# Performance work log

Measured on AMD Instinct MI355X. Metric: run time of the kernel, lower is better.

Reference implementation:

```python
import jax, jax.numpy as jnp
import numpy as np

DIM = 1024
HEADS = 16
DIM_HEAD = 64
INNER = HEADS * DIM_HEAD  # 1024
B, N = 2, 2048


def setup_inputs() -> dict:
    key = jax.random.key(0)
    ks = jax.random.split(key, 8)
    q = jax.random.normal(ks[0], (B, N, DIM), dtype=jnp.float32)
    k = jax.random.normal(ks[1], (B, N, DIM), dtype=jnp.float32)
    v = jax.random.normal(ks[2], (B, N, DIM), dtype=jnp.float32)
    # True = masked out (masked_fill semantics); causal mask broadcast over batch
    causal = jnp.triu(jnp.ones((N, N), dtype=jnp.bool_), k=1)
    mask = jnp.broadcast_to(causal, (B, N, N))
    s = 0.02
    Wq = jax.random.normal(ks[3], (DIM, INNER), dtype=jnp.float32) * s
    Wk = jax.random.normal(ks[4], (DIM, INNER), dtype=jnp.float32) * s
    Wv = jax.random.normal(ks[5], (DIM, INNER), dtype=jnp.float32) * s
    Wo = jax.random.normal(ks[6], (INNER, DIM), dtype=jnp.float32) * s
    bo = jnp.zeros((DIM,), dtype=jnp.float32)
    return {"q": q, "k": k, "v": v, "mask": mask,
            "Wq": Wq, "Wk": Wk, "Wv": Wv, "Wo": Wo, "bo": bo}


def reference(q, k, v, mask, Wq, Wk, Wv, Wo, bo):
    h, d = HEADS, DIM_HEAD
    scale = d ** -0.5
    b, n, _ = q.shape

    def heads_split(x):  # [b, n, h*d] -> [b, h, n, d]
        return x.reshape(b, -1, h, d).transpose(0, 2, 1, 3)

    qh = heads_split(q @ Wq)
    kh = heads_split(k @ Wk)
    vh = heads_split(v @ Wv)

    dots = jnp.einsum('bhid,bhjd->bhij', qh, kh) * scale  # [b,h,n,n]
    mask_value = -jnp.finfo(dots.dtype).max
    dots = jnp.where(mask[:, None, :, :], mask_value, dots)
    attn = jax.nn.softmax(dots, axis=-1)
    out = jnp.einsum('bhij,bhjd->bhid', attn, vh)          # [b,h,n,d]
    out = out.transpose(0, 2, 1, 3).reshape(b, n, h * d)    # [b,n,h*d]
    out = out @ Wo + bo                                     # RowParallelLinear (bias=True)
    return out  # dropout p=0.0 is identity
```

## Files before the change

### kernel.cpp

```cpp
#include <hip/hip_runtime.h>

typedef __attribute__((ext_vector_type(8))) short short8;
typedef __attribute__((ext_vector_type(4))) float f32x4;
typedef __attribute__((ext_vector_type(4))) unsigned int u32x4;

#define MFMA_BF16(a, b, c) __builtin_amdgcn_mfma_f32_16x16x32_bf16((a), (b), (c), 0, 0, 0)

#define GLOAD16(g, l) __builtin_amdgcn_global_load_lds( \
    (const __attribute__((address_space(1))) void*)(g),  \
    (__attribute__((address_space(3))) void*)(l), 16, 0, 0)

#define BARRIER() __builtin_amdgcn_s_barrier()
#define LGKMCNT0() do { asm volatile("s_waitcnt lgkmcnt(0)" ::: "memory"); \
                        __builtin_amdgcn_sched_barrier(0); } while (0)
#define VMCNT(n) asm volatile("s_waitcnt vmcnt(" n ")" ::: "memory")

static __device__ __forceinline__ unsigned short f2bf(float f) {
    unsigned int u = __builtin_bit_cast(unsigned int, f);
    u += 0x7fffu + ((u >> 16) & 1u);
    return (unsigned short)(u >> 16);
}
static __device__ __forceinline__ unsigned int cvtpk(float a, float b) {
    unsigned int r;
    asm("v_cvt_pk_bf16_f32 %0, %1, %2" : "=v"(r) : "v"(a), "v"(b));
    return r;
}
static __device__ __forceinline__ float ex2(float x) {
    float r;
    asm("v_exp_f32 %0, %1" : "=v"(r) : "v"(x));
    return r;
}

__global__ __launch_bounds__(256) void convX_kernel(
    const float* __restrict__ q, const float* __restrict__ k, const float* __restrict__ v,
    unsigned short* __restrict__ dq, unsigned short* __restrict__ dk,
    unsigned short* __restrict__ dv)
{
    const float* s; unsigned short* d;
    switch (blockIdx.y) {
        case 0:  s = q; d = dq; break;
        case 1:  s = k; d = dk; break;
        default: s = v; d = dv; break;
    }
    int i = (blockIdx.x * 256 + threadIdx.x) * 8;
    float4 a = *reinterpret_cast<const float4*>(s + i);
    float4 b = *reinterpret_cast<const float4*>(s + i + 4);
    short8 o;
    o[0] = (short)f2bf(a.x); o[1] = (short)f2bf(a.y);
    o[2] = (short)f2bf(a.z); o[3] = (short)f2bf(a.w);
    o[4] = (short)f2bf(b.x); o[5] = (short)f2bf(b.y);
    o[6] = (short)f2bf(b.z); o[7] = (short)f2bf(b.w);
    *reinterpret_cast<short8*>(d + i) = o;
}

__global__ __launch_bounds__(256) void convWT_kernel(
    const float* __restrict__ w0, const float* __restrict__ w1,
    const float* __restrict__ w2, const float* __restrict__ w3,
    unsigned short* __restrict__ t0, unsigned short* __restrict__ t1,
    unsigned short* __restrict__ t2, unsigned short* __restrict__ t3)
{
    const float* W; unsigned short* T;
    switch (blockIdx.z) {
        case 0:  W = w0; T = t0; break;
        case 1:  W = w1; T = t1; break;
        case 2:  W = w2; T = t2; break;
        default: W = w3; T = t3; break;
    }
    __shared__ unsigned short ldsT[64][72];
    const int t = threadIdx.x;
    const int kb = blockIdx.x * 64, cb = blockIdx.y * 64;

    const int c4 = (t & 15) * 4;
    const int r0 = t >> 4;
    #pragma unroll
    for (int i = 0; i < 4; ++i) {
        int kr = r0 + i * 16;
        float4 wv = *reinterpret_cast<const float4*>(&W[(size_t)(kb + kr) * 1024 + cb + c4]);
        ldsT[c4 + 0][kr] = f2bf(wv.x);
        ldsT[c4 + 1][kr] = f2bf(wv.y);
        ldsT[c4 + 2][kr] = f2bf(wv.z);
        ldsT[c4 + 3][kr] = f2bf(wv.w);
    }
    __syncthreads();
    const int c = t >> 2;
    const int kp = (t & 3) * 16;
    short8 o0 = *reinterpret_cast<const short8*>(&ldsT[c][kp]);
    short8 o1 = *reinterpret_cast<const short8*>(&ldsT[c][kp + 8]);
    *reinterpret_cast<short8*>(&T[(size_t)(cb + c) * 1024 + kb + kp])     = o0;
    *reinterpret_cast<short8*>(&T[(size_t)(cb + c) * 1024 + kb + kp + 8]) = o1;
}

__device__ __forceinline__ void gemm_body(
    const unsigned short* __restrict__ A, const unsigned short* __restrict__ B,
    int tm, int cn, unsigned short* Al, unsigned short* Bl, f32x4 acc[4][4])
{
    const int t = threadIdx.x;
    const int lane = t & 63, w = t >> 6;
    const int lr = lane & 15, lg = lane >> 4;
    const int wr = w >> 1, wc = w & 1;

    const int srow = w * 16 + (lane >> 2);
    const int sk   = (lane & 3) * 8;
    const unsigned short* ga = A + (size_t)(tm + srow) * 1024 + sk;
    const unsigned short* gb = B + (size_t)(cn + srow) * 1024 + sk;
    unsigned short* la = Al + srow * 32 + sk;
    unsigned short* lb = Bl + srow * 32 + sk;

    for (int k0 = 0; k0 < 1024; k0 += 32) {
        __syncthreads();
        GLOAD16(ga + k0, la);
        GLOAD16(ga + k0 + (size_t)64 * 1024, la + 64 * 32);
        GLOAD16(gb + k0, lb);
        GLOAD16(gb + k0 + (size_t)64 * 1024, lb + 64 * 32);
        asm volatile("s_waitcnt vmcnt(0)" ::: "memory");
        __syncthreads();

        short8 af[4], bfr[4];
        #pragma unroll
        for (int i = 0; i < 4; ++i) {
            af[i]  = *reinterpret_cast<const short8*>(&Al[(wr * 64 + i * 16 + lr) * 32 + lg * 8]);
            bfr[i] = *reinterpret_cast<const short8*>(&Bl[(wc * 64 + i * 16 + lr) * 32 + lg * 8]);
        }
        #pragma unroll
        for (int mi = 0; mi < 4; ++mi)
            #pragma unroll
            for (int ni = 0; ni < 4; ++ni)
                acc[mi][ni] = MFMA_BF16(af[mi], bfr[ni], acc[mi][ni]);
    }
}

__global__ __launch_bounds__(512, 2) void qkv_gemm(
    const unsigned short* __restrict__ Xq, const unsigned short* __restrict__ Xk,
    const unsigned short* __restrict__ Xv,
    const unsigned short* __restrict__ WqT, const unsigned short* __restrict__ WkT,
    const unsigned short* __restrict__ WvT,
    unsigned short* __restrict__ Qh, unsigned short* __restrict__ Kh,
    unsigned short* __restrict__ VhT)
{
    extern __shared__ unsigned short lds[];
    const int t    = threadIdx.x;
    const int lane = t & 63, w = t >> 6;
    const int lr   = lane & 15, lg = lane >> 4;
    const int wrow = w >> 2, wcol = w & 3;
    const int sw   = lr & 7;

    const int z = blockIdx.z;
    const unsigned short *A, *B; unsigned short* dst;
    int tm, cn;
    if (z == 2)      { A = WvT; B = Xv;  dst = VhT; tm = blockIdx.y * 256; cn = blockIdx.x * 256; }
    else if (z == 1) { A = Xk;  B = WkT; dst = Kh;  tm = blockIdx.x * 256; cn = blockIdx.y * 256; }
    else             { A = Xq;  B = WqT; dst = Qh;  tm = blockIdx.x * 256; cn = blockIdx.y * 256; }

    const unsigned short* Ag = A + (size_t)tm * 1024;
    const unsigned short* Bg = B + (size_t)cn * 1024;

    const int sr    = t >> 3;
    const int gsw   = (t & 7) ^ (sr & 7);
    const int brow0 = (sr >> 5) * 64 + (sr & 31);

    auto stageA = [&](int q, int kt, unsigned short* slabA) {
        const unsigned short* g = Ag + (size_t)(q * 64 + sr) * 1024 + kt + gsw * 8;
        GLOAD16(g, slabA + q * 8192 + t * 8);
        GLOAD16(g + (size_t)128 * 1024, slabA + q * 8192 + 4096 + t * 8);
    };
    auto stageB = [&](int s, int kt, unsigned short* slabB) {
        const unsigned short* g = Bg + (size_t)(brow0 + s * 32) * 1024 + kt + gsw * 8;
        GLOAD16(g, slabB + s * 8192 + t * 8);
        GLOAD16(g + (size_t)128 * 1024, slabB + s * 8192 + 4096 + t * 8);
    };

    short8 rA[4][2], rB0[2][2], rB1[2][2];
    auto ldA = [&](const unsigned short* bufA, int q) {
        #pragma unroll
        for (int m2 = 0; m2 < 4; ++m2) {
            const unsigned short* p = bufA + q * 8192 + (wrow * 64 + m2 * 16 + lr) * 64;
            rA[m2][0] = *reinterpret_cast<const short8*>(p + (lg ^ sw) * 8);
            rA[m2][1] = *reinterpret_cast<const short8*>(p + ((4 + lg) ^ sw) * 8);
        }
    };
    auto ldB = [&](const unsigned short* bufB, int s, short8 rB[2][2]) {
        #pragma unroll
        for (int n2 = 0; n2 < 2; ++n2) {
            const unsigned short* p = bufB + s * 8192 + (wcol * 32 + n2 * 16 + lr) * 64;
            rB[n2][0] = *reinterpret_cast<const short8*>(p + (lg ^ sw) * 8);
            rB[n2][1] = *reinterpret_cast<const short8*>(p + ((4 + lg) ^ sw) * 8);
        }
    };

    f32x4 acc[8][4];
    #pragma unroll
    for (int i = 0; i < 8; ++i)
        #pragma unroll
        for (int j = 0; j < 4; ++j) acc[i][j] = (f32x4){0.f, 0.f, 0.f, 0.f};

#define QUAD(MH, NH, RB) do {                                            \
    _Pragma("unroll")                                                    \
    for (int m2 = 0; m2 < 4; ++m2) {                                     \
        _Pragma("unroll")                                                \
        for (int n2 = 0; n2 < 2; ++n2) {                                 \
            f32x4 c_ = acc[(MH)*4 + m2][(NH)*2 + n2];                    \
            c_ = MFMA_BF16(rA[m2][0], (RB)[n2][0], c_);                  \
            c_ = MFMA_BF16(rA[m2][1], (RB)[n2][1], c_);                  \
            acc[(MH)*4 + m2][(NH)*2 + n2] = c_;                          \
        } } } while (0)

    stageA(0, 0, lds);
    stageB(0, 0, lds + 16384);
    stageB(1, 0, lds + 16384);
    stageA(1, 0, lds);
    VMCNT("4");
    BARRIER();

    for (int tt = 0; tt < 15; ++tt) {
        unsigned short* cA = lds + (tt & 1) * 32768;
        unsigned short* cB = cA + 16384;
        unsigned short* nA = lds + ((tt + 1) & 1) * 32768;
        unsigned short* nB = nA + 16384;
        const int kn = (tt + 1) * 64;
        stageA(0, kn, nA);
        ldA(cA, 0); ldB(cB, 0, rB0);
        VMCNT("4"); BARRIER(); LGKMCNT0();
        __builtin_amdgcn_s_setprio(1); QUAD(0, 0, rB0); __builtin_amdgcn_s_setprio(0);
        BARRIER();
        stageB(0, kn, nB);
        ldB(cB, 1, rB1);
        VMCNT("4"); BARRIER(); LGKMCNT0();
        __builtin_amdgcn_s_setprio(1); QUAD(0, 1, rB1); __builtin_amdgcn_s_setprio(0);
        BARRIER();
        stageB(1, kn, nB);
        ldA(cA, 1);
        BARRIER(); LGKMCNT0();
        __builtin_amdgcn_s_setprio(1); QUAD(1, 1, rB1); __builtin_amdgcn_s_setprio(0);
        BARRIER();
        stageA(1, kn, nA);
        VMCNT("4"); BARRIER(); LGKMCNT0();
        __builtin_amdgcn_s_setprio(1); QUAD(1, 0, rB0); __builtin_amdgcn_s_setprio(0);
        BARRIER();
    }
    {
        unsigned short* cA = lds + 32768;
        unsigned short* cB = cA + 16384;
        ldA(cA, 0); ldB(cB, 0, rB0);
        VMCNT("2"); BARRIER(); LGKMCNT0();
        __builtin_amdgcn_s_setprio(1); QUAD(0, 0, rB0); __builtin_amdgcn_s_setprio(0);
        BARRIER();
        ldB(cB, 1, rB1);
        VMCNT("0"); BARRIER(); LGKMCNT0();
        __builtin_amdgcn_s_setprio(1); QUAD(0, 1, rB1); __builtin_amdgcn_s_setprio(0);
        BARRIER();
        ldA(cA, 1);
        LGKMCNT0();
        __builtin_amdgcn_s_setprio(1); QUAD(1, 1, rB1); QUAD(1, 0, rB0);
        __builtin_amdgcn_s_setprio(0);
    }
#undef QUAD

    if (z == 2) {
        #pragma unroll
        for (int mi = 0; mi < 8; ++mi)
            #pragma unroll
            for (int ni = 0; ni < 4; ++ni)
                #pragma unroll
                for (int r = 0; r < 4; ++r) {
                    int c    = tm + wrow * 128 + mi * 16 + lg * 4 + r;
                    int nseq = cn + wcol * 64 + ni * 16 + lr;
                    int b = nseq >> 11, n = nseq & 2047;
                    int h = c >> 6, d = c & 63;
                    dst[(((size_t)(b * 16 + h) * 64 + d) << 11) + n] = f2bf(acc[mi][ni][r]);
                }
    } else {
        const float sc = (z == 0) ? 0.18033688011112042f : 1.0f;
        #pragma unroll
        for (int mi = 0; mi < 8; ++mi)
            #pragma unroll
            for (int ni = 0; ni < 4; ++ni)
                #pragma unroll
                for (int r = 0; r < 4; ++r) {
                    int orow = tm + wrow * 128 + mi * 16 + lg * 4 + r;
                    int ocol = cn + wcol * 64 + ni * 16 + lr;
                    int b = orow >> 11, n = orow & 2047;
                    int h = ocol >> 6, d = ocol & 63;
                    dst[(((size_t)(b * 16 + h) * 2048 + n) << 6) + d] = f2bf(acc[mi][ni][r] * sc);
                }
    }
}

__global__ __launch_bounds__(256) void o_gemm(
    const unsigned short* __restrict__ Ctx, const unsigned short* __restrict__ WoT,
    const float* __restrict__ bias, float* __restrict__ out)
{
    __shared__ unsigned short Al[128 * 32];
    __shared__ unsigned short Bl[128 * 32];
    const int tm = blockIdx.x * 128, cn = blockIdx.y * 128;

    f32x4 acc[4][4];
    #pragma unroll
    for (int i = 0; i < 4; ++i)
        #pragma unroll
        for (int j = 0; j < 4; ++j) acc[i][j] = (f32x4){0.f, 0.f, 0.f, 0.f};

    gemm_body(Ctx, WoT, tm, cn, Al, Bl, acc);

    const int lane = threadIdx.x & 63, w = threadIdx.x >> 6;
    const int lr = lane & 15, lg = lane >> 4;
    const int wr = w >> 1, wc = w & 1;

    #pragma unroll
    for (int mi = 0; mi < 4; ++mi)
        #pragma unroll
        for (int ni = 0; ni < 4; ++ni)
            #pragma unroll
            for (int r = 0; r < 4; ++r) {
                int orow = tm + wr * 64 + mi * 16 + lg * 4 + r;
                int ocol = cn + wc * 64 + ni * 16 + lr;
                out[(size_t)orow * 1024 + ocol] = acc[mi][ni][r] + bias[ocol];
            }
}

__global__ __launch_bounds__(256, 2) void attn_kernel(
    const unsigned short* __restrict__ Qh, const unsigned short* __restrict__ Kh,
    const unsigned short* __restrict__ VhT, unsigned short* __restrict__ Ctx)
{
    __shared__ unsigned short KV[3][8192];

    const int t  = threadIdx.x;
    const int l  = t & 63, w = t >> 6;
    const int lr = l & 15, lg = l >> 4;
    const int rg = w & 1, jh = w >> 1;
    const int swz = lr & 7;

    const int lin  = blockIdx.x;
    const int xcd  = lin & 7;
    const int j    = lin >> 3;
    const int bh   = xcd * 4 + (j & 3);
    const int u    = j >> 2;
    const int strip = (u & 1) ? (u >> 1) : (31 - (u >> 1));
    const int b    = bh >> 4, h = bh & 15;

    const unsigned short* Qb = Qh  + (size_t)bh * (2048 * 64);
    const unsigned short* Kb = Kh  + (size_t)bh * (2048 * 64);
    const unsigned short* Vb = VhT + (size_t)bh * (64 * 2048);

    const int srow = t >> 3;
    const int sg   = (t & 7) ^ (srow & 7);

    auto stage = [&](int jt, int bf) {
        const unsigned short* kg0 = Kb + (size_t)(jt + srow) * 64 + sg * 8;
        unsigned short* kl = &KV[bf][0] + w * 512;
        GLOAD16(kg0, kl);
        GLOAD16(kg0 + 32 * 64, kl + 2048);
        const unsigned short* vg0 = Vb + (size_t)srow * 2048 + jt + sg * 8;
        unsigned short* vl = &KV[bf][4096] + w * 512;
        GLOAD16(vg0, vl);
        GLOAD16(vg0 + (size_t)32 * 2048, vl + 2048);
    };

    const int qbase = strip * 64 + rg * 32;
    const int ns    = strip + 1;

    short8 bQ[2][2];
    #pragma unroll
    for (int qg = 0; qg < 2; ++qg) {
        const unsigned short* qp = Qb + (size_t)(qbase + qg * 16 + lr) * 64 + lg * 8;
        bQ[qg][0] = *reinterpret_cast<const short8*>(qp);
        bQ[qg][1] = *reinterpret_cast<const short8*>(qp + 32);
    }

    f32x4 acc[2][4];
    #pragma unroll
    for (int qg = 0; qg < 2; ++qg)
        #pragma unroll
        for (int di = 0; di < 4; ++di) acc[qg][di] = (f32x4){0.f, 0.f, 0.f, 0.f};
    float lsum[2] = {0.f, 0.f};

    stage(0, 0);
    if (ns > 1) stage(64, 1);

    int cur = 0;
    for (int s = 0; s < ns; ++s) {
        if (s + 1 < ns) { VMCNT("4"); } else { VMCNT("0"); }
        BARRIER();
        __builtin_amdgcn_sched_barrier(0);
        if (s + 2 < ns) {
            int nb = cur + 2; if (nb >= 3) nb -= 3;
            stage(64 * (s + 2), nb);
        }

        const int jt = 64 * s + jh * 32;
        const unsigned short* Ks = &KV[cur][0];
        const unsigned short* Vs = &KV[cur][4096];

        short8 aK[2][2];
        #pragma unroll
        for (int kg = 0; kg < 2; ++kg) {
            const int rT = jh * 32 + kg * 16 + lr;
            aK[kg][0] = *reinterpret_cast<const short8*>(Ks + rT * 64 + ((lg ^ swz) << 3));
            aK[kg][1] = *reinterpret_cast<const short8*>(Ks + rT * 64 + (((4 + lg) ^ swz) << 3));
        }
        short8 bV[4];
        #pragma unroll
        for (int di = 0; di < 4; ++di) {
            const int d = lr + 16 * di;
            bV[di] = *reinterpret_cast<const short8*>(Vs + d * 64 + (((jh * 4 + lg) ^ swz) << 3));
        }

        f32x4 sf[2][2];
        __builtin_amdgcn_s_setprio(1);
        #pragma unroll
        for (int kg = 0; kg < 2; ++kg)
            #pragma unroll
            for (int qg = 0; qg < 2; ++qg) {
                f32x4 z = (f32x4){0.f, 0.f, 0.f, 0.f};
                z = MFMA_BF16(aK[kg][0], bQ[qg][0], z);
                sf[kg][qg] = MFMA_BF16(aK[kg][1], bQ[qg][1], z);
            }
        __builtin_amdgcn_s_setprio(0);

        #pragma unroll
        for (int qg = 0; qg < 2; ++qg) {
            const int qrow = qbase + qg * 16 + lr;
            float p[8];
            if (jt + 31 > qbase + qg * 16) {
                #pragma unroll
                for (int r = 0; r < 4; ++r) {
                    p[r]     = (jt + lg * 4 + r      > qrow) ? 0.f : ex2(sf[0][qg][r]);
                    p[4 + r] = (jt + 16 + lg * 4 + r > qrow) ? 0.f : ex2(sf[1][qg][r]);
                }
            } else {
                #pragma unroll
                for (int r = 0; r < 4; ++r) {
                    p[r] = ex2(sf[0][qg][r]); p[4 + r] = ex2(sf[1][qg][r]);
                }
            }

            lsum[qg] += (p[0] + p[1]) + (p[2] + p[3]) + (p[4] + p[5]) + (p[6] + p[7]);

            unsigned int c0 = cvtpk(p[0], p[1]);
            unsigned int c1 = cvtpk(p[2], p[3]);
            unsigned int c2 = cvtpk(p[4], p[5]);
            unsigned int c3 = cvtpk(p[6], p[7]);
            asm("v_permlane32_swap_b32 %0, %1" : "+v"(c0), "+v"(c2));
            asm("v_permlane32_swap_b32 %0, %1" : "+v"(c1), "+v"(c3));
            asm("v_permlane16_swap_b32 %0, %1" : "+v"(c0), "+v"(c2));
            asm("v_permlane16_swap_b32 %0, %1" : "+v"(c1), "+v"(c3));
            short8 aP = __builtin_bit_cast(short8, (u32x4){c0, c1, c2, c3});

            __builtin_amdgcn_s_setprio(1);
            #pragma unroll
            for (int di = 0; di < 4; ++di)
                acc[qg][di] = MFMA_BF16(aP, bV[di], acc[qg][di]);
            __builtin_amdgcn_s_setprio(0);
        }

        cur = (cur + 1 == 3) ? 0 : cur + 1;
    }

    #pragma unroll
    for (int qg = 0; qg < 2; ++qg) {
        lsum[qg] += __shfl_xor(lsum[qg], 16);
        lsum[qg] += __shfl_xor(lsum[qg], 32);
    }

    __syncthreads();

    float* cmb = (float*)&KV[0][0];
    if (jh == 1) {
        float* cp = cmb + (size_t)(rg * 64 + l) * 36;
        #pragma unroll
        for (int qg = 0; qg < 2; ++qg)
            #pragma unroll
            for (int di = 0; di < 4; ++di)
                *reinterpret_cast<f32x4*>(cp + (qg * 4 + di) * 4) = acc[qg][di];
        cp[32] = lsum[0]; cp[33] = lsum[1];
    }
    __syncthreads();
    if (jh == 0) {
        const float* cp = cmb + (size_t)(rg * 64 + l) * 36;
        #pragma unroll
        for (int qg = 0; qg < 2; ++qg) {
            #pragma unroll
            for (int di = 0; di < 4; ++di)
                acc[qg][di] += *reinterpret_cast<const f32x4*>(cp + (qg * 4 + di) * 4);
            float lt = lsum[qg] + cp[32 + qg];
            float linv[4];
            #pragma unroll
            for (int r = 0; r < 4; ++r) linv[r] = 1.f / __shfl(lt, lg * 4 + r);
            #pragma unroll
            for (int di = 0; di < 4; ++di) {
                #pragma unroll
                for (int r = 0; r < 4; ++r) {
                    int row = qbase + qg * 16 + lg * 4 + r;
                    Ctx[(size_t)(b * 2048 + row) * 1024 + h * 64 + di * 16 + lr] =
                        f2bf(acc[qg][di][r] * linv[r]);
                }
            }
        }
    }
}

extern "C" void kernel_launch(void* const* d_in, const int* in_sizes, int n_in,
                              void* d_out, int out_size, void* d_ws, size_t ws_size,
                              hipStream_t stream) {
    const float* q  = (const float*)d_in[0];
    const float* k  = (const float*)d_in[1];
    const float* v  = (const float*)d_in[2];
    const float* Wq = (const float*)d_in[4];
    const float* Wk = (const float*)d_in[5];
    const float* Wv = (const float*)d_in[6];
    const float* Wo = (const float*)d_in[7];
    const float* bo = (const float*)d_in[8];
    float* out = (float*)d_out;

    const size_t HSZ = (size_t)32 * 2048 * 64;
    const size_t WSZ = (size_t)1024 * 1024;
    unsigned short* Qh  = (unsigned short*)d_ws;
    unsigned short* Kh  = Qh + HSZ;
    unsigned short* VhT = Kh + HSZ;
    unsigned short* Xqb = VhT + HSZ;
    unsigned short* Xkb = Xqb + HSZ;
    unsigned short* Xvb = Xkb + HSZ;
    unsigned short* WqT = Xvb + HSZ;
    unsigned short* WkT = WqT + WSZ;
    unsigned short* WvT = WkT + WSZ;
    unsigned short* WoT = WvT + WSZ;
    unsigned short* Ctx = Xqb;

    hipFuncSetAttribute(reinterpret_cast<const void*>(qkv_gemm),
                        hipFuncAttributeMaxDynamicSharedMemorySize, 131072);

    dim3 blk(256);
    convX_kernel<<<dim3(2048, 3), blk, 0, stream>>>(q, k, v, Xqb, Xkb, Xvb);
    convWT_kernel<<<dim3(16, 16, 4), blk, 0, stream>>>(Wq, Wk, Wv, Wo, WqT, WkT, WvT, WoT);
    qkv_gemm<<<dim3(16, 4, 3), dim3(512), 131072, stream>>>(Xqb, Xkb, Xvb, WqT, WkT, WvT, Qh, Kh, VhT);
    attn_kernel<<<dim3(1024), blk, 0, stream>>>(Qh, Kh, VhT, Ctx);
    o_gemm<<<dim3(32, 8), blk, 0, stream>>>(Ctx, WoT, bo, out);
}
```

Before: 108.0 us.

## Triple-buffer o_gemm LDS loads to overlap global fetches with MFMA

Replaces the single-buffered o_gemm mainloop, which waited on vmcnt(0) before every k-step, with a three-stage LDS ring. The next two k-tiles are prefetched via global_load_lds while the current one is consumed, with one barrier per step. It also raises wave priority around the MFMA block. This hides global load latency but triples o_gemm shared memory, which may reduce occupancy.

Measured after the change: 102.0 us. 5.5% less time.

```diff
diff --git a/kernel.cpp b/kernel.cpp
--- a/kernel.cpp
+++ b/kernel.cpp
@@ -88,45 +88,6 @@
     short8 o1 = *reinterpret_cast<const short8*>(&ldsT[c][kp + 8]);
     *reinterpret_cast<short8*>(&T[(size_t)(cb + c) * 1024 + kb + kp])     = o0;
     *reinterpret_cast<short8*>(&T[(size_t)(cb + c) * 1024 + kb + kp + 8]) = o1;
-}
-
-__device__ __forceinline__ void gemm_body(
-    const unsigned short* __restrict__ A, const unsigned short* __restrict__ B,
-    int tm, int cn, unsigned short* Al, unsigned short* Bl, f32x4 acc[4][4])
-{
-    const int t = threadIdx.x;
-    const int lane = t & 63, w = t >> 6;
-    const int lr = lane & 15, lg = lane >> 4;
-    const int wr = w >> 1, wc = w & 1;
-
-    const int srow = w * 16 + (lane >> 2);
-    const int sk   = (lane & 3) * 8;
-    const unsigned short* ga = A + (size_t)(tm + srow) * 1024 + sk;
-    const unsigned short* gb = B + (size_t)(cn + srow) * 1024 + sk;
-    unsigned short* la = Al + srow * 32 + sk;
-    unsigned short* lb = Bl + srow * 32 + sk;
-
-    for (int k0 = 0; k0 < 1024; k0 += 32) {
-        __syncthreads();
-        GLOAD16(ga + k0, la);
-        GLOAD16(ga + k0 + (size_t)64 * 1024, la + 64 * 32);
-        GLOAD16(gb + k0, lb);
-        GLOAD16(gb + k0 + (size_t)64 * 1024, lb + 64 * 32);
-        asm volatile("s_waitcnt vmcnt(0)" ::: "memory");
-        __syncthreads();
-
-        short8 af[4], bfr[4];
-        #pragma unroll
-        for (int i = 0; i < 4; ++i) {
-            af[i]  = *reinterpret_cast<const short8*>(&Al[(wr * 64 + i * 16 + lr) * 32 + lg * 8]);
-            bfr[i] = *reinterpret_cast<const short8*>(&Bl[(wc * 64 + i * 16 + lr) * 32 + lg * 8]);
-        }
-        #pragma unroll
-        for (int mi = 0; mi < 4; ++mi)
-            #pragma unroll
-            for (int ni = 0; ni < 4; ++ni)
-                acc[mi][ni] = MFMA_BF16(af[mi], bfr[ni], acc[mi][ni]);
-    }
 }
 
 __global__ __launch_bounds__(512, 2) void qkv_gemm(
@@ -289,21 +250,61 @@
     const unsigned short* __restrict__ Ctx, const unsigned short* __restrict__ WoT,
     const float* __restrict__ bias, float* __restrict__ out)
 {
-    __shared__ unsigned short Al[128 * 32];
-    __shared__ unsigned short Bl[128 * 32];
-    const int tm = blockIdx.x * 128, cn = blockIdx.y * 128;
-
-    f32x4 acc[4][4];
-    #pragma unroll
-    for (int i = 0; i < 4; ++i)
-        #pragma unroll
-        for (int j = 0; j < 4; ++j) acc[i][j] = (f32x4){0.f, 0.f, 0.f, 0.f};
-
-    gemm_body(Ctx, WoT, tm, cn, Al, Bl, acc);
-
-    const int lane = threadIdx.x & 63, w = threadIdx.x >> 6;
+    __shared__ unsigned short LB[3][8192];
+    const int t = threadIdx.x;
+    const int lane = t & 63, w = t >> 6;
     const int lr = lane & 15, lg = lane >> 4;
     const int wr = w >> 1, wc = w & 1;
+    const int tm = blockIdx.x * 128, cn = blockIdx.y * 128;
+
+    const int srow = w * 16 + (lane >> 2);
+    const int sk   = (lane & 3) * 8;
+    const unsigned short* ga = Ctx + (size_t)(tm + srow) * 1024 + sk;
+    const unsigned short* gb = WoT + (size_t)(cn + srow) * 1024 + sk;
+    const int lo = srow * 32 + sk;
+
+    auto stage = [&](int k0, int bf) {
+        GLOAD16(ga + k0, &LB[bf][lo]);
+        GLOAD16(ga + k0 + (size_t)64 * 1024, &LB[bf][64 * 32 + lo]);
+        GLOAD16(gb + k0, &LB[bf][4096 + lo]);
+        GLOAD16(gb + k0 + (size_t)64 * 1024, &LB[bf][4096 + 64 * 32 + lo]);
+    };
+
+    f32x4 acc[4][4];
+    #pragma unroll
+    for (int i = 0; i < 4; ++i)
+        #pragma unroll
+        for (int j = 0; j < 4; ++j) acc[i][j] = (f32x4){0.f, 0.f, 0.f, 0.f};
+
+    stage(0, 0);
+    stage(32, 1);
+
+    int cur = 0;
+    for (int s = 0; s < 32; ++s) {
+        if (s + 1 < 32) { VMCNT("4"); } else { VMCNT("0"); }
+        BARRIER();
+        __builtin_amdgcn_sched_barrier(0);
+        if (s + 2 < 32) {
+            int nb = cur + 2; if (nb >= 3) nb -= 3;
+            stage(32 * (s + 2), nb);
+        }
+
+        short8 af[4], bfr[4];
+        #pragma unroll
+        for (int i = 0; i < 4; ++i) {
+            af[i]  = *reinterpret_cast<const short8*>(&LB[cur][(wr * 64 + i * 16 + lr) * 32 + lg * 8]);
+            bfr[i] = *reinterpret_cast<const short8*>(&LB[cur][4096 + (wc * 64 + i * 16 + lr) * 32 + lg * 8]);
+        }
+        __builtin_amdgcn_s_setprio(1);
+        #pragma unroll
+        for (int mi = 0; mi < 4; ++mi)
+            #pragma unroll
+            for (int ni = 0; ni < 4; ++ni)
+                acc[mi][ni] = MFMA_BF16(af[mi], bfr[ni], acc[mi][ni]);
+        __builtin_amdgcn_s_setprio(0);
+
+        cur = (cur + 1 == 3) ? 0 : cur + 1;
+    }
 
     #pragma unroll
     for (int mi = 0; mi < 4; ++mi)
```
